# Kernel tuning notes

Hardware: AMD Instinct MI355X
Metric: run time of the kernel (lower is better)

Reference implementation:

```python
import jax, jax.numpy as jnp
import numpy as np

# Config mirroring MultiHeadAttention1d(in_channels=256, n_heads=8, residual=False,
# kernel_size=1, attention_type=0) applied to 3-D inputs (B, C, N).
B, C, N, H, D = 4, 256, 2048, 8, 256  # per-head dim D = in_channels; OC = H*D = 2048
OC = H * D


def setup_inputs() -> dict:
    key = jax.random.key(0)
    ks = jax.random.split(key, 14)
    s = 1.0 / np.sqrt(C)
    f32 = jnp.float32
    inp = {
        "x": jax.random.normal(ks[0], (B, C, N), f32),
        "y": jax.random.normal(ks[1], (B, C, N), f32),
        # ConvNormActivation1d (kernel_size=1) == pointwise conv + (folded, eval-mode)
        # BatchNorm affine + ReLU. BN folds to per-channel scale g and shift beta.
        "Wq": jax.random.normal(ks[2], (OC, C), f32) * s,
        "bq": jax.random.normal(ks[3], (OC,), f32) * 0.01,
        "gq": jnp.ones((OC,), f32),
        "betaq": jnp.zeros((OC,), f32),
        "Wk": jax.random.normal(ks[4], (OC, C), f32) * s,
        "bk": jax.random.normal(ks[5], (OC,), f32) * 0.01,
        "gk": jnp.ones((OC,), f32),
        "betak": jnp.zeros((OC,), f32),
        "Wv": jax.random.normal(ks[6], (OC, C), f32) * s,
        "bv": jax.random.normal(ks[7], (OC,), f32) * 0.01,
        "gv": jnp.ones((OC,), f32),
        "betav": jnp.zeros((OC,), f32),
    }
    return inp


def _cna(W, b, g, beta, t):
    # 1x1 conv (channel GEMM) + folded-BN affine + ReLU; t: (B, C, N) -> (B, OC, N)
    z = jnp.einsum("oc,bcn->bon", W, t) + b[:, None]
    return jax.nn.relu(g[:, None] * z + beta[:, None])


def _heads(t):
    # (B, OC, N) -> (B, H, N, D); channel split matches torch.split chunks of size D
    return t.reshape(B, H, D, N).transpose(0, 1, 3, 2)


def reference(x, y, Wq, bq, gq, betaq, Wk, bk, gk, betak, Wv, bv, gv, betav):
    q = _heads(_cna(Wq, bq, gq, betaq, x))  # (B,H,N,D)
    k = _heads(_cna(Wk, bk, gk, betak, y))
    v = _heads(_cna(Wv, bv, gv, betav, y))
    energy = jnp.einsum("bhnd,bhmd->bhnm", q, k)  # bmm(Q, K^T)
    attn = jax.nn.softmax(energy, axis=-1)
    out = jnp.einsum("bhnm,bhmd->bhnd", attn, v)  # (B,H,N,D)
    # torch path: view(H,B,k,N,D).permute(1,0,3,2,4) -> (B,H,N,k=1,D);
    # squeeze(dim=2) is a no-op since N != 1.
    return out[:, :, :, None, :]  # (B, H, N, 1, D)
```

## Files before the change

### kernel.cpp

```cpp
#include <hip/hip_runtime.h>
#include <cstdint>
#include <cstddef>

typedef unsigned short u16;
typedef __attribute__((ext_vector_type(4))) float f32x4;
typedef __attribute__((ext_vector_type(16))) float f32x16;
typedef __attribute__((ext_vector_type(8))) _Float16 f16x8;
typedef __attribute__((ext_vector_type(4))) u16   u16x4;
typedef __attribute__((ext_vector_type(8))) u16   u16x8;
typedef __attribute__((ext_vector_type(4))) int   i32x4;

#define DEV static __device__ __forceinline__
#define MFMA16(a,b,c) __builtin_amdgcn_mfma_f32_16x16x32_f16((a),(b),(c),0,0,0)
#define MFMA32(a,b,c) __builtin_amdgcn_mfma_f32_32x32x16_f16((a),(b),(c),0,0,0)

constexpr int Bc = 4, Cc = 256, Nc = 2048, Hc = 8, Dc = 256, OCc = 2048;

constexpr size_t OFF_XT = 0;
constexpr size_t OFF_YT = OFF_XT + (size_t)Bc*Nc*Cc*2;
constexpr size_t OFF_WQ = OFF_YT + (size_t)Bc*Nc*Cc*2;
constexpr size_t OFF_WK = OFF_WQ + (size_t)OCc*Cc*2;
constexpr size_t OFF_WV = OFF_WK + (size_t)OCc*Cc*2;
constexpr size_t OFF_BQ = OFF_WV + (size_t)OCc*Cc*2;
constexpr size_t OFF_BK = OFF_BQ + (size_t)OCc*4;
constexpr size_t OFF_BV = OFF_BK + (size_t)OCc*4;
constexpr size_t OFF_Q  = OFF_BV + (size_t)OCc*4;
constexpr size_t OFF_K  = OFF_Q  + (size_t)Bc*Hc*Nc*Dc*2;
constexpr size_t OFF_V  = OFF_K  + (size_t)Bc*Hc*Nc*Dc*2;

DEV u16 f2h(float x){
  _Float16 h = (_Float16)x;
  return __builtin_bit_cast(u16, h);
}

DEV void load_lds16(const void* g, void* l){
  __builtin_amdgcn_global_load_lds((const __attribute__((address_space(1))) int*)g,
                                   (__attribute__((address_space(3))) int*)l, 16, 0, 0);
}

__global__ __launch_bounds__(256) void transpose_cast(const float* __restrict__ x,
                                                      const float* __restrict__ y,
                                                      u16* __restrict__ XT,
                                                      u16* __restrict__ YT){
  __shared__ u16 tile[64][65];
  int b = blockIdx.z >> 1;
  const float* src = (blockIdx.z & 1) ? y : x;
  u16* dst = (blockIdx.z & 1) ? YT : XT;
  int n0 = blockIdx.x * 64, c0 = blockIdx.y * 64;
  int t = threadIdx.x;
#pragma unroll
  for (int i = 0; i < 16; ++i){
    int slot = i*256 + t;
    int cl = slot >> 6, nl = slot & 63;
    tile[cl][nl] = f2h(src[((size_t)b*Cc + c0 + cl)*Nc + n0 + nl]);
  }
  __syncthreads();
#pragma unroll
  for (int i = 0; i < 8; ++i){
    int slot = i*256 + t;
    int nl = slot >> 5, cl = (slot & 31)*2;
    uint32_t v = (uint32_t)tile[cl][nl] | ((uint32_t)tile[cl+1][nl] << 16);
    *(uint32_t*)(dst + ((size_t)b*Nc + n0 + nl)*Cc + c0 + cl) = v;
  }
}

__global__ __launch_bounds__(256) void prep_w(const float* __restrict__ W,
                                              const float* __restrict__ bsrc,
                                              const float* __restrict__ g,
                                              const float* __restrict__ beta,
                                              u16* __restrict__ Wo,
                                              float* __restrict__ bb){
  int idx = (blockIdx.x*256 + threadIdx.x) * 8;
  int o = idx >> 8, c = idx & 255;
  float gg = g[o];
  f32x4 a0 = *(const f32x4*)(W + idx);
  f32x4 a1 = *(const f32x4*)(W + idx + 4);
  u16x8 r;
#pragma unroll
  for (int i = 0; i < 4; ++i){ r[i] = f2h(a0[i]*gg); r[i+4] = f2h(a1[i]*gg); }
  *(u16x8*)(Wo + idx) = r;
  if (c == 0) bb[o] = gg*bsrc[o] + beta[o];
}

template<int SW>
__global__ __launch_bounds__(256, 2) void proj_gemm(const u16* __restrict__ Xt,
                                                    const u16* __restrict__ Wp,
                                                    const float* __restrict__ bb,
                                                    u16* __restrict__ outp){
  __shared__ __align__(16) char lds[32768];
  int t = threadIdx.x, w = t >> 6, l = t & 63, q = l & 15, g = l >> 4;
  int b = blockIdx.z;
  int n0 = blockIdx.x * 128, o0 = blockIdx.y * 128;
  int fs = ((q >> 1) & 3) << 4;
  int partg = ((l & 3) ^ ((l >> 3) & 3));
  f32x4 acc[4][4] = {};

  for (int it = 0; it < 4; ++it){
    __syncthreads();
#pragma unroll
    for (int j = 0; j < 8; ++j){
      int s = j*4 + w;
      int chunk = s >> 3;
      int off = (s & 7) * 1024;
      int row = (s & 7)*16 + (l >> 2);
      const char* gsrc;
      if (chunk < 2)
        gsrc = (const char*)(Wp + (size_t)(o0 + row)*Cc) + it*128 + chunk*64 + partg*16;
      else
        gsrc = (const char*)(Xt + ((size_t)b*Nc + n0 + row)*Cc) + it*128 + (chunk & 1)*64 + partg*16;
      load_lds16(gsrc, lds + chunk*8192 + off);
    }
    asm volatile("s_waitcnt vmcnt(0)" ::: "memory");
    __syncthreads();
#pragma unroll
    for (int kc = 0; kc < 2; ++kc){
      f16x8 fw[4], fx[4];
#pragma unroll
      for (int i = 0; i < 4; ++i){
        int wrow = (SW ? (w & 1) : (w >> 1))*64 + i*16 + q;
        int xrow = (SW ? (w >> 1) : (w & 1))*64 + i*16 + q;
        fw[i] = *(const f16x8*)(lds + kc*8192 + wrow*64 + ((g*16) ^ fs));
        fx[i] = *(const f16x8*)(lds + 16384 + kc*8192 + xrow*64 + ((g*16) ^ fs));
      }
#pragma unroll
      for (int i = 0; i < 4; ++i)
#pragma unroll
        for (int jj = 0; jj < 4; ++jj){
          if constexpr (!SW) acc[i][jj] = MFMA16(fw[i], fx[jj], acc[i][jj]);
          else               acc[i][jj] = MFMA16(fx[i], fw[jj], acc[i][jj]);
        }
    }
  }

  if constexpr (!SW) {
    f32x4 bias[4];
#pragma unroll
    for (int i = 0; i < 4; ++i) bias[i] = *(const f32x4*)(bb + o0 + (w>>1)*64 + i*16 + 4*g);
#pragma unroll
    for (int i = 0; i < 4; ++i)
#pragma unroll
      for (int jj = 0; jj < 4; ++jj){
        u16x4 pk;
#pragma unroll
        for (int r = 0; r < 4; ++r){
          float z = acc[i][jj][r] + bias[i][r];
          pk[r] = f2h(fmaxf(z, 0.f));
        }
        int o = o0 + (w>>1)*64 + i*16 + 4*g;
        int n = n0 + (w&1)*64 + jj*16 + q;
        int hh = o >> 8, d = o & 255;
        *(u16x4*)(outp + ((size_t)((b*Hc + hh)*Nc + n))*Dc + d) = pk;
      }
  } else {
    float biasv[4];
#pragma unroll
    for (int i = 0; i < 4; ++i) biasv[i] = bb[o0 + (w&1)*64 + i*16 + q];
#pragma unroll
    for (int i = 0; i < 4; ++i)
#pragma unroll
      for (int jj = 0; jj < 4; ++jj){
        u16x4 pk;
#pragma unroll
        for (int r = 0; r < 4; ++r){
          float z = acc[i][jj][r] + biasv[jj];
          pk[r] = f2h(fmaxf(z, 0.f));
        }
        int o = o0 + (w&1)*64 + jj*16 + q;
        int n = n0 + (w>>1)*64 + i*16 + 4*g;
        int hh = o >> 8, d = o & 255;
        *(u16x4*)(outp + ((size_t)((b*Hc + hh)*Dc + d))*Nc + n) = pk;
      }
  }
}

__global__ __launch_bounds__(256, 2) void attn_kernel(const u16* __restrict__ Qp,
                                                      const u16* __restrict__ Kp,
                                                      const u16* __restrict__ Vp,
                                                      float* __restrict__ outp){
  __shared__ __align__(16) char lds[58880];
  const int t = threadIdx.x, w = t >> 6, l = t & 63, lq = l & 31, hi = l >> 5;
  const int wq = w & 1, wm = w >> 1;
  const int h = blockIdx.y, b = blockIdx.z;
  const int q0 = blockIdx.x * 64;
  size_t head = (size_t)(b*Hc + h) * Nc * Dc;
  const u16* Qh = Qp + head;
  const u16* Kh = Kp + head;
  const u16* Vh = Vp + head;

  char* Kl = lds;
  char* Vl = lds + 32768;
  char* Px = lds + 49152;
  float* smax = (float*)(lds + 57344);
  float* ssum = (float*)(lds + 57856);
  float* sscl = (float*)(lds + 58368);
  float* slinv= (float*)(lds + 58624);

  f16x8 qf[16];
  {
    const u16* qrow = Qh + (size_t)(q0 + wq*32 + lq) * Dc;
#pragma unroll
    for (int kc = 0; kc < 16; ++kc) qf[kc] = *(const f16x8*)(qrow + kc*16 + hi*8);
  }

  f32x16 acc[4] = {};
  float m_run = -1e30f, l_run = 0.f;

  for (int kv = 0; kv < 32; ++kv){
    const int m0 = kv * 64;
    __syncthreads();
#pragma unroll
    for (int j = 0; j < 8; ++j){
      int row = w*16 + j*2 + hi;
      int gs = (l & 31) ^ (row & 7);
      load_lds16(Kh + (size_t)(m0 + row)*Dc + gs*8, Kl + w*8192 + j*1024);
    }
#pragma unroll
    for (int j = 0; j < 4; ++j){
      int ri = w*4 + j;
      int rd = ri*16 + (l >> 2);
      int gs = (l & 3) ^ (rd & 3);
      load_lds16(Vh + (size_t)rd*Nc + m0 + gs*8, Vl + ri*1024);
    }
    asm volatile("s_waitcnt vmcnt(0)" ::: "memory");
    __syncthreads();

    f32x16 s = {};
#pragma unroll
    for (int kc = 0; kc < 16; ++kc){
      f16x8 kf = *(const f16x8*)(Kl + (wm*32 + lq)*512 + ((kc*32 + hi*16) ^ ((l & 7) << 4)));
      s = MFMA32(kf, qf[kc], s);
    }

    float tmax = s[0];
#pragma unroll
    for (int r = 1; r < 16; ++r) tmax = fmaxf(tmax, s[r]);
    tmax = fmaxf(tmax, __shfl_xor(tmax, 32));
    if (!hi) smax[(wq*2 + wm)*32 + lq] = tmax;
    __syncthreads();
    float omax = smax[(wq*2 + (1 - wm))*32 + lq];
    float mnew = fmaxf(m_run, fmaxf(tmax, omax));
    float scale = __expf(m_run - mnew);

    float p[16];
    float rsum = 0.f;
#pragma unroll
    for (int r = 0; r < 16; ++r){ p[r] = __expf(s[r] - mnew); rsum += p[r]; }
    rsum += __shfl_xor(rsum, 32);
    if (!hi){
      ssum[(wq*2 + wm)*32 + lq] = rsum;
      if (!wm) sscl[wq*32 + lq] = scale;
    }

    int pk[8];
#pragma unroll
    for (int j2 = 0; j2 < 8; ++j2)
      pk[j2] = __builtin_bit_cast(int, __builtin_amdgcn_cvt_pkrtz(p[2*j2], p[2*j2+1]));
    int sx[8];
#pragma unroll
    for (int j2 = 0; j2 < 8; ++j2) sx[j2] = __shfl_xor(pk[j2], 32);
    i32x4 f0, f1;
    f0[0] = hi ? sx[2] : pk[0];  f0[1] = hi ? sx[3] : pk[1];
    f0[2] = hi ? pk[2] : sx[0];  f0[3] = hi ? pk[3] : sx[1];
    f1[0] = hi ? sx[6] : pk[4];  f1[1] = hi ? sx[7] : pk[5];
    f1[2] = hi ? pk[6] : sx[4];  f1[3] = hi ? pk[7] : sx[5];
    *(i32x4*)(Px + w*2048 + l*16)        = f0;
    *(i32x4*)(Px + w*2048 + 1024 + l*16) = f1;
    __syncthreads();

    float osum = ssum[(wq*2 + (1 - wm))*32 + lq];
    l_run = l_run * scale + rsum + osum;
    m_run = mnew;

    float sc[16];
#pragma unroll
    for (int r = 0; r < 16; ++r) sc[r] = sscl[wq*32 + (r & 3) + 8*(r >> 2) + 4*hi];
#pragma unroll
    for (int dt = 0; dt < 4; ++dt)
#pragma unroll
      for (int r = 0; r < 16; ++r) acc[dt][r] *= sc[r];

    i32x4 g0 = *(const i32x4*)(Px + (w ^ 2)*2048 + l*16);
    i32x4 g1 = *(const i32x4*)(Px + (w ^ 2)*2048 + 1024 + l*16);
    f16x8 a0 = __builtin_bit_cast(f16x8, wm ? g0 : f0);
    f16x8 a1 = __builtin_bit_cast(f16x8, wm ? g1 : f1);
    f16x8 a2 = __builtin_bit_cast(f16x8, wm ? f0 : g0);
    f16x8 a3 = __builtin_bit_cast(f16x8, wm ? f1 : g1);

#pragma unroll
    for (int dt = 0; dt < 4; ++dt)
#pragma unroll
      for (int mcl = 0; mcl < 2; ++mcl){
        f16x8 vf = *(const f16x8*)(Vl + (wm*128 + dt*32 + lq)*64 + (((mcl*2 + hi)*16) ^ ((l & 3) << 4)));
        acc[dt] = MFMA32(mcl ? a1 : a0, vf, acc[dt]);
      }
    __syncthreads();
#pragma unroll
    for (int j = 0; j < 4; ++j){
      int ri = w*4 + j;
      int rd = ri*16 + (l >> 2);
      int gs = (l & 3) ^ (rd & 3);
      load_lds16(Vh + (size_t)rd*Nc + m0 + 32 + gs*8, Vl + ri*1024);
    }
    asm volatile("s_waitcnt vmcnt(0)" ::: "memory");
    __syncthreads();
#pragma unroll
    for (int dt = 0; dt < 4; ++dt)
#pragma unroll
      for (int mcl = 0; mcl < 2; ++mcl){
        f16x8 vf = *(const f16x8*)(Vl + (wm*128 + dt*32 + lq)*64 + (((mcl*2 + hi)*16) ^ ((l & 3) << 4)));
        acc[dt] = MFMA32(mcl ? a3 : a2, vf, acc[dt]);
      }
  }

  if (!hi && !wm) slinv[wq*32 + lq] = 1.f / l_run;
  __syncthreads();
  float li[16];
#pragma unroll
  for (int r = 0; r < 16; ++r) li[r] = slinv[wq*32 + (r & 3) + 8*(r >> 2) + 4*hi];
#pragma unroll
  for (int dt = 0; dt < 4; ++dt)
#pragma unroll
    for (int r = 0; r < 16; ++r){
      int qrow_ = wq*32 + (r & 3) + 8*(r >> 2) + 4*hi;
      int d = wm*128 + dt*32 + lq;
      outp[head + (size_t)(q0 + qrow_)*Dc + d] = acc[dt][r] * li[r];
    }
}

extern "C" void kernel_launch(void* const* d_in, const int* in_sizes, int n_in,
                              void* d_out, int out_size, void* d_ws, size_t ws_size,
                              hipStream_t stream){
  const float* x     = (const float*)d_in[0];
  const float* y     = (const float*)d_in[1];
  const float* Wq    = (const float*)d_in[2];
  const float* bq    = (const float*)d_in[3];
  const float* gq    = (const float*)d_in[4];
  const float* betaq = (const float*)d_in[5];
  const float* Wk    = (const float*)d_in[6];
  const float* bk    = (const float*)d_in[7];
  const float* gk    = (const float*)d_in[8];
  const float* betak = (const float*)d_in[9];
  const float* Wv    = (const float*)d_in[10];
  const float* bv    = (const float*)d_in[11];
  const float* gv    = (const float*)d_in[12];
  const float* betav = (const float*)d_in[13];
  char* ws = (char*)d_ws;
  float* outp = (float*)d_out;

  u16* XT = (u16*)(ws + OFF_XT);
  u16* YT = (u16*)(ws + OFF_YT);
  u16* WQb = (u16*)(ws + OFF_WQ);
  u16* WKb = (u16*)(ws + OFF_WK);
  u16* WVb = (u16*)(ws + OFF_WV);
  float* BQ = (float*)(ws + OFF_BQ);
  float* BK = (float*)(ws + OFF_BK);
  float* BV = (float*)(ws + OFF_BV);
  u16* Qw = (u16*)(ws + OFF_Q);
  u16* Kw = (u16*)(ws + OFF_K);
  u16* Vw = (u16*)(ws + OFF_V);

  transpose_cast<<<dim3(Nc/64, Cc/64, Bc*2), 256, 0, stream>>>(x, y, XT, YT);
  prep_w<<<dim3(OCc*Cc/2048), 256, 0, stream>>>(Wq, bq, gq, betaq, WQb, BQ);
  prep_w<<<dim3(OCc*Cc/2048), 256, 0, stream>>>(Wk, bk, gk, betak, WKb, BK);
  prep_w<<<dim3(OCc*Cc/2048), 256, 0, stream>>>(Wv, bv, gv, betav, WVb, BV);

  dim3 pg(Nc/128, OCc/128, Bc);
  proj_gemm<0><<<pg, 256, 0, stream>>>(XT, WQb, BQ, Qw);
  proj_gemm<0><<<pg, 256, 0, stream>>>(YT, WKb, BK, Kw);
  proj_gemm<1><<<pg, 256, 0, stream>>>(YT, WVb, BV, Vw);

  attn_kernel<<<dim3(Nc/64, Hc, Bc), 256, 0, stream>>>(Qw, Kw, Vw, outp);
}
```

Before: 307.8 us.

## Double-buffer K/V tiles in LDS with 128-query, 8-wave attention blocks

The attention kernel now uses 512-thread blocks covering 128 query rows, so each K/V tile staged in LDS is shared by twice as many queries. K and the full 64-column V tile are double-buffered: the next tile is loaded while the current one is consumed. This replaces the old split V load with its extra barriers. MFMA sections are wrapped in s_setprio to favour matrix issue. The cost is about 147 KB of LDS per block, which allows only one block per CU and leaves less room for scheduling slack.

```diff
diff --git a/kernel.cpp b/kernel.cpp
--- a/kernel.cpp
+++ b/kernel.cpp
@@ -173,27 +173,25 @@
   }
 }
 
-__global__ __launch_bounds__(256, 2) void attn_kernel(const u16* __restrict__ Qp,
+__global__ __launch_bounds__(512, 1) void attn_kernel(const u16* __restrict__ Qp,
                                                       const u16* __restrict__ Kp,
                                                       const u16* __restrict__ Vp,
                                                       float* __restrict__ outp){
-  __shared__ __align__(16) char lds[58880];
+  __shared__ __align__(16) char lds[150528];
   const int t = threadIdx.x, w = t >> 6, l = t & 63, lq = l & 31, hi = l >> 5;
-  const int wq = w & 1, wm = w >> 1;
+  const int wq = w & 3, wm = w >> 2;
   const int h = blockIdx.y, b = blockIdx.z;
-  const int q0 = blockIdx.x * 64;
+  const int q0 = blockIdx.x * 128;
   size_t head = (size_t)(b*Hc + h) * Nc * Dc;
   const u16* Qh = Qp + head;
   const u16* Kh = Kp + head;
   const u16* Vh = Vp + head;
 
-  char* Kl = lds;
-  char* Vl = lds + 32768;
-  char* Px = lds + 49152;
-  float* smax = (float*)(lds + 57344);
-  float* ssum = (float*)(lds + 57856);
-  float* sscl = (float*)(lds + 58368);
-  float* slinv= (float*)(lds + 58624);
+  char* Pex  = lds + 131072;
+  float* smax = (float*)(lds + 147456);
+  float* ssum = (float*)(lds + 148480);
+  float* sscl = (float*)(lds + 149504);
+  float* slinv= (float*)(lds + 150016);
 
   f16x8 qf[16];
   {
@@ -205,31 +203,44 @@
   f32x16 acc[4] = {};
   float m_run = -1e30f, l_run = 0.f;
 
-  for (int kv = 0; kv < 32; ++kv){
-    const int m0 = kv * 64;
-    __syncthreads();
-#pragma unroll
-    for (int j = 0; j < 8; ++j){
-      int row = w*16 + j*2 + hi;
-      int gs = (l & 31) ^ (row & 7);
-      load_lds16(Kh + (size_t)(m0 + row)*Dc + gs*8, Kl + w*8192 + j*1024);
-    }
-#pragma unroll
-    for (int j = 0; j < 4; ++j){
-      int ri = w*4 + j;
-      int rd = ri*16 + (l >> 2);
-      int gs = (l & 3) ^ (rd & 3);
-      load_lds16(Vh + (size_t)rd*Nc + m0 + gs*8, Vl + ri*1024);
-    }
-    asm volatile("s_waitcnt vmcnt(0)" ::: "memory");
-    __syncthreads();
+#define STAGE_KV(m0_, buf_)                                                        \
+  {                                                                                \
+    char* Kd = lds + (buf_)*32768;                                                 \
+    char* Vd = lds + 65536 + (buf_)*32768;                                         \
+    _Pragma("unroll")                                                              \
+    for (int j = 0; j < 4; ++j){                                                   \
+      int row = w*8 + j*2 + hi;                                                    \
+      int gs = (l & 31) ^ (row & 7);                                               \
+      load_lds16(Kh + (size_t)((m0_) + row)*Dc + gs*8, Kd + w*4096 + j*1024);      \
+    }                                                                              \
+    _Pragma("unroll")                                                              \
+    for (int j = 0; j < 4; ++j){                                                   \
+      int ri = w*4 + j;                                                            \
+      int rd = ri*8 + (l >> 3);                                                    \
+      int gs = (l & 7) ^ (rd & 7);                                                 \
+      load_lds16(Vh + (size_t)rd*Nc + (m0_) + gs*8, Vd + ri*1024 + l*16);          \
+    }                                                                              \
+  }
+
+  STAGE_KV(0, 0);
+  asm volatile("s_waitcnt vmcnt(0)" ::: "memory");
+  __syncthreads();
+
+  for (int it = 0; it < 32; ++it){
+    const int cur = it & 1;
+    char* Kc = lds + cur*32768;
+    char* Vc = lds + 65536 + cur*32768;
+
+    if (it < 31) STAGE_KV((it + 1)*64, cur ^ 1);
 
     f32x16 s = {};
+    __builtin_amdgcn_s_setprio(1);
 #pragma unroll
     for (int kc = 0; kc < 16; ++kc){
-      f16x8 kf = *(const f16x8*)(Kl + (wm*32 + lq)*512 + ((kc*32 + hi*16) ^ ((l & 7) << 4)));
+      f16x8 kf = *(const f16x8*)(Kc + (wm*32 + lq)*512 + ((kc*32 + hi*16) ^ ((l & 7) << 4)));
       s = MFMA32(kf, qf[kc], s);
     }
+    __builtin_amdgcn_s_setprio(0);
 
     float tmax = s[0];
 #pragma unroll
@@ -263,8 +274,8 @@
     f0[2] = hi ? pk[2] : sx[0];  f0[3] = hi ? pk[3] : sx[1];
     f1[0] = hi ? sx[6] : pk[4];  f1[1] = hi ? sx[7] : pk[5];
     f1[2] = hi ? pk[6] : sx[4];  f1[3] = hi ? pk[7] : sx[5];
-    *(i32x4*)(Px + w*2048 + l*16)        = f0;
-    *(i32x4*)(Px + w*2048 + 1024 + l*16) = f1;
+    *(i32x4*)(Pex + w*2048 + l*16)        = f0;
+    *(i32x4*)(Pex + w*2048 + 1024 + l*16) = f1;
     __syncthreads();
 
     float osum = ssum[(wq*2 + (1 - wm))*32 + lq];
@@ -279,38 +290,31 @@
 #pragma unroll
       for (int r = 0; r < 16; ++r) acc[dt][r] *= sc[r];
 
-    i32x4 g0 = *(const i32x4*)(Px + (w ^ 2)*2048 + l*16);
-    i32x4 g1 = *(const i32x4*)(Px + (w ^ 2)*2048 + 1024 + l*16);
+    i32x4 g0 = *(const i32x4*)(Pex + (w ^ 4)*2048 + l*16);
+    i32x4 g1 = *(const i32x4*)(Pex + (w ^ 4)*2048 + 1024 + l*16);
     f16x8 a0 = __builtin_bit_cast(f16x8, wm ? g0 : f0);
     f16x8 a1 = __builtin_bit_cast(f16x8, wm ? g1 : f1);
     f16x8 a2 = __builtin_bit_cast(f16x8, wm ? f0 : g0);
     f16x8 a3 = __builtin_bit_cast(f16x8, wm ? f1 : g1);
 
-#pragma unroll
-    for (int dt = 0; dt < 4; ++dt)
-#pragma unroll
-      for (int mcl = 0; mcl < 2; ++mcl){
-        f16x8 vf = *(const f16x8*)(Vl + (wm*128 + dt*32 + lq)*64 + (((mcl*2 + hi)*16) ^ ((l & 3) << 4)));
-        acc[dt] = MFMA32(mcl ? a1 : a0, vf, acc[dt]);
-      }
-    __syncthreads();
-#pragma unroll
-    for (int j = 0; j < 4; ++j){
-      int ri = w*4 + j;
-      int rd = ri*16 + (l >> 2);
-      int gs = (l & 3) ^ (rd & 3);
-      load_lds16(Vh + (size_t)rd*Nc + m0 + 32 + gs*8, Vl + ri*1024);
-    }
+    __builtin_amdgcn_s_setprio(1);
+#pragma unroll
+    for (int h2 = 0; h2 < 2; ++h2)
+#pragma unroll
+      for (int dt = 0; dt < 4; ++dt)
+#pragma unroll
+        for (int mcl = 0; mcl < 2; ++mcl){
+          f16x8 vf = *(const f16x8*)(Vc + (wm*128 + dt*32 + lq)*128 +
+                                     (((h2*4 + mcl*2 + hi)*16) ^ ((l & 7) << 4)));
+          f16x8 af = h2 ? (mcl ? a3 : a2) : (mcl ? a1 : a0);
+          acc[dt] = MFMA32(af, vf, acc[dt]);
+        }
+    __builtin_amdgcn_s_setprio(0);
+
     asm volatile("s_waitcnt vmcnt(0)" ::: "memory");
     __syncthreads();
-#pragma unroll
-    for (int dt = 0; dt < 4; ++dt)
-#pragma unroll
-      for (int mcl = 0; mcl < 2; ++mcl){
-        f16x8 vf = *(const f16x8*)(Vl + (wm*128 + dt*32 + lq)*64 + (((mcl*2 + hi)*16) ^ ((l & 3) << 4)));
-        acc[dt] = MFMA32(mcl ? a3 : a2, vf, acc[dt]);
-      }
-  }
+  }
+#undef STAGE_KV
 
   if (!hi && !wm) slinv[wq*32 + lq] = 1.f / l_run;
   __syncthreads();
@@ -369,5 +373,5 @@
   proj_gemm<0><<<pg, 256, 0, stream>>>(YT, WKb, BK, Kw);
   proj_gemm<1><<<pg, 256, 0, stream>>>(YT, WVb, BV, Vw);
 
-  attn_kernel<<<dim3(Nc/64, Hc, Bc), 256, 0, stream>>>(Qw, Kw, Vw, outp);
-}
+  attn_kernel<<<dim3(Nc/128, Hc, Bc), 512, 0, stream>>>(Qw, Kw, Vw, outp);
+}
```

Measured after the change: 270.8 us. 1.14x faster.
